# Kernel optimization log

Measured on AMD Instinct MI355X. Metric: run time of the kernel, lower is better.

## Reference

```python
import jax, jax.numpy as jnp
import numpy as np

I_SIZE, H_SIZE, O_SIZE = 3, 128, 3
B, T, A = 512, 50, 64


def _xavier(k, shape):
    fan_out, fan_in = shape
    limit = float(np.sqrt(6.0 / (fan_in + fan_out)))
    return jax.random.uniform(k, shape, minval=-limit, maxval=limit, dtype=jnp.float32)


def setup_inputs() -> dict:
    key = jax.random.key(0)
    ks = jax.random.split(key, 6)
    src = jax.random.normal(ks[0], (B, T, A * I_SIZE), dtype=jnp.float32)
    return {
        "src": src,
        "W_ih_enc": _xavier(ks[1], (H_SIZE, I_SIZE)),
        "W_hh_enc": _xavier(ks[2], (H_SIZE, H_SIZE)),
        "b_ih_enc": jnp.zeros((H_SIZE,), jnp.float32),
        "b_hh_enc": jnp.zeros((H_SIZE,), jnp.float32),
        "W_ih_dec": _xavier(ks[3], (H_SIZE, O_SIZE)),
        "W_hh_dec": _xavier(ks[4], (H_SIZE, H_SIZE)),
        "b_ih_dec": jnp.zeros((H_SIZE,), jnp.float32),
        "b_hh_dec": jnp.zeros((H_SIZE,), jnp.float32),
        "fc_W": _xavier(ks[5], (O_SIZE, H_SIZE)),
        "fc_b": jnp.zeros((O_SIZE,), jnp.float32),
        "pred_len": 12,
    }


def reference(src, W_ih_enc, W_hh_enc, b_ih_enc, b_hh_enc,
              W_ih_dec, W_hh_dec, b_ih_dec, b_hh_dec, fc_W, fc_b, pred_len):
    b, t, f = src.shape
    a = f // I_SIZE
    # (b, t, a*I) -> (t, b*a, I): agents batched together (vectorizes the per-agent loop)
    xs = src.reshape(b, t, a, I_SIZE).transpose(1, 0, 2, 3).reshape(t, b * a, I_SIZE)

    def enc_step(h, x_t):
        h = jnp.tanh(x_t @ W_ih_enc.T + b_ih_enc + h @ W_hh_enc.T + b_hh_enc)
        return h, None

    h0 = jnp.zeros((b * a, H_SIZE), src.dtype)
    h_enc, _ = jax.lax.scan(enc_step, h0, xs)

    # decoder input = last observed position of each agent
    dec_in0 = xs[-1]  # (b*a, I)

    def dec_step(carry, _):
        h, inp = carry
        h = jnp.tanh(inp @ W_ih_dec.T + b_ih_dec + h @ W_hh_dec.T + b_hh_dec)
        pred = h @ fc_W.T + fc_b  # (b*a, O)
        return (h, pred), pred

    _, preds = jax.lax.scan(dec_step, (h_enc, dec_in0), None, length=pred_len)
    # (pred_len, b*a, O) -> (b, pred_len, a*O)
    out = preds.reshape(pred_len, b, a, O_SIZE).transpose(1, 0, 2, 3).reshape(b, pred_len, a * O_SIZE)
    return out
```

## Files before the change

### kernel.cpp

```cpp
#include <hip/hip_runtime.h>
#include <stdint.h>

typedef _Float16 f16x8 __attribute__((ext_vector_type(8)));
typedef float f32x4 __attribute__((ext_vector_type(4)));
typedef unsigned int u32x4 __attribute__((ext_vector_type(4)));

#define T_OBS 50
#define PRED 12

#define DEC_OFF 20480
#define FC_OFF  40960
#define WS_ELEMS 43008

__device__ __forceinline__ int unperm(int k) {
  return (k & 3) | (((k >> 3) & 3) << 2) | (((k >> 2) & 1) << 4) | (k & 0x60);
}

__global__ void prep_kernel(const float* __restrict__ Wih_e, const float* __restrict__ Whh_e,
                            const float* __restrict__ bih_e, const float* __restrict__ bhh_e,
                            const float* __restrict__ Wih_d, const float* __restrict__ Whh_d,
                            const float* __restrict__ bih_d, const float* __restrict__ bhh_d,
                            const float* __restrict__ fcW,
                            unsigned short* __restrict__ ws) {
  int idx = blockIdx.x * 256 + threadIdx.x;
  if (idx >= WS_ELEMS) return;
  float val = 0.0f;
  if (idx < FC_OFF) {
    const bool enc = idx < DEC_OFF;
    const int e = enc ? idx : idx - DEC_OFF;
    const int j = e & 7;
    const int lane = (e >> 3) & 63;
    const int rem = e >> 9;
    const int kt = rem % 5;
    const int t = rem / 5;
    const int n = 16 * t + (lane & 15);
    const int kappa = 32 * kt + ((lane >> 4) << 3) + j;
    const float* Wih = enc ? Wih_e : Wih_d;
    const float* Whh = enc ? Whh_e : Whh_d;
    const float* bih = enc ? bih_e : bih_d;
    const float* bhh = enc ? bhh_e : bhh_d;
    if (kappa < 128)       val = Whh[n * 128 + unperm(kappa)];
    else if (kappa < 131)  val = Wih[n * 3 + (kappa - 128)];
    else if (kappa == 131) val = bih[n] + bhh[n];
  } else {
    const int e = idx - FC_OFF;
    const int j = e & 7;
    const int lane = (e >> 3) & 63;
    const int kt = e >> 9;
    const int o = lane & 15;
    const int kappa = 32 * kt + ((lane >> 4) << 3) + j;
    if (o < 3) val = fcW[o * 128 + unperm(kappa)];
  }
  _Float16 h = (_Float16)val;
  ws[idx] = __builtin_bit_cast(unsigned short, h);
}

__device__ __forceinline__ float tanh_fast(float v) {
  float e = __builtin_amdgcn_exp2f(v * 2.8853900817779268f);
  return __builtin_fmaf(-2.0f, __builtin_amdgcn_rcpf(1.0f + e), 1.0f);
}

__device__ __forceinline__ unsigned int pk2(float a, float b) {
  return __builtin_bit_cast(unsigned int, __builtin_amdgcn_cvt_pkrtz(a, b));
}

__device__ __forceinline__ f16x8 ldfrag(const unsigned short* p) {
  return __builtin_bit_cast(f16x8, *(const u32x4*)p);
}

__device__ __forceinline__ f16x8 mkxf(float a, float b, float c) {
  u32x4 u;
  u[0] = pk2(a, b);
  u[1] = pk2(c, 1.0f);
  u[2] = 0u;
  u[3] = 0u;
  return __builtin_bit_cast(f16x8, u);
}

__global__ __launch_bounds__(256, 3) void traj_kernel(
    const float* __restrict__ src, const unsigned short* __restrict__ ws,
    const float* __restrict__ fcb, float* __restrict__ out) {
  __shared__ unsigned short xch[2][4][2][64][8];

  const int lane = (int)(threadIdx.x & 63u);
  const int w = (int)(threadIdx.x >> 6u);
  const int l15 = lane & 15;
  const int sA = blockIdx.x * 32 + l15;
  const int sB = sA + 16;
  const float* xpA = src + (size_t)(sA >> 6) * (T_OBS * 192) + (sA & 63) * 3;
  const float* xpB = src + (size_t)(sB >> 6) * (T_OBS * 192) + (sB & 63) * 3;

  f16x8 A0[5], A1[5];
  #pragma unroll
  for (int i = 0; i < 5; ++i) {
    const int kt = (i < 4) ? ((w + i) & 3) : 4;
    A0[i] = ldfrag(ws + (size_t)(((2 * w)     * 5 + kt) * 64 + lane) * 8);
    A1[i] = ldfrag(ws + (size_t)(((2 * w + 1) * 5 + kt) * 64 + lane) * 8);
  }

  f16x8 B0[4], B1[4];
  #pragma unroll
  for (int i = 0; i < 4; ++i) {
    u32x4 zz = (u32x4)0u;
    B0[i] = __builtin_bit_cast(f16x8, zz);
    B1[i] = __builtin_bit_cast(f16x8, zz);
  }

  f16x8 xf0 = mkxf(xpA[0], xpA[1], xpA[2]);
  f16x8 xf1 = mkxf(xpB[0], xpB[1], xpB[2]);

  auto rnn_step = [&](int par, f16x8 xfa, f16x8 xfb) {
    const f32x4 z = (f32x4){0.f, 0.f, 0.f, 0.f};
    f32x4 aA = __builtin_amdgcn_mfma_f32_16x16x32_f16(A0[4], xfa, z, 0, 0, 0);
    f32x4 aB = __builtin_amdgcn_mfma_f32_16x16x32_f16(A1[4], xfa, z, 0, 0, 0);
    f32x4 aC = __builtin_amdgcn_mfma_f32_16x16x32_f16(A0[4], xfb, z, 0, 0, 0);
    f32x4 aD = __builtin_amdgcn_mfma_f32_16x16x32_f16(A1[4], xfb, z, 0, 0, 0);
    #pragma unroll
    for (int i = 0; i < 4; ++i) {
      aA = __builtin_amdgcn_mfma_f32_16x16x32_f16(A0[i], B0[i], aA, 0, 0, 0);
      aB = __builtin_amdgcn_mfma_f32_16x16x32_f16(A1[i], B0[i], aB, 0, 0, 0);
      aC = __builtin_amdgcn_mfma_f32_16x16x32_f16(A0[i], B1[i], aC, 0, 0, 0);
      aD = __builtin_amdgcn_mfma_f32_16x16x32_f16(A1[i], B1[i], aD, 0, 0, 0);
    }
    u32x4 F0, F1;
    F0[0] = pk2(tanh_fast(aA[0]), tanh_fast(aA[1]));
    F0[1] = pk2(tanh_fast(aA[2]), tanh_fast(aA[3]));
    F0[2] = pk2(tanh_fast(aB[0]), tanh_fast(aB[1]));
    F0[3] = pk2(tanh_fast(aB[2]), tanh_fast(aB[3]));
    F1[0] = pk2(tanh_fast(aC[0]), tanh_fast(aC[1]));
    F1[1] = pk2(tanh_fast(aC[2]), tanh_fast(aC[3]));
    F1[2] = pk2(tanh_fast(aD[0]), tanh_fast(aD[1]));
    F1[3] = pk2(tanh_fast(aD[2]), tanh_fast(aD[3]));
    *(u32x4*)&xch[par][w][0][lane][0] = F0;
    *(u32x4*)&xch[par][w][1][lane][0] = F1;
    __syncthreads();
    B0[0] = __builtin_bit_cast(f16x8, F0);
    B1[0] = __builtin_bit_cast(f16x8, F1);
    #pragma unroll
    for (int i = 1; i < 4; ++i) {
      B0[i] = ldfrag(&xch[par][(w + i) & 3][0][lane][0]);
      B1[i] = ldfrag(&xch[par][(w + i) & 3][1][lane][0]);
    }
  };

  for (int s = 0; s < T_OBS; ++s) {
    const int t2 = (s < T_OBS - 1) ? s + 1 : s;
    const float na0 = xpA[t2 * 192], na1 = xpA[t2 * 192 + 1], na2 = xpA[t2 * 192 + 2];
    const float nb0 = xpB[t2 * 192], nb1 = xpB[t2 * 192 + 1], nb2 = xpB[t2 * 192 + 2];
    rnn_step(s & 1, xf0, xf1);
    xf0 = mkxf(na0, na1, na2);
    xf1 = mkxf(nb0, nb1, nb2);
  }

  #pragma unroll
  for (int i = 0; i < 5; ++i) {
    const int kt = (i < 4) ? ((w + i) & 3) : 4;
    A0[i] = ldfrag(ws + DEC_OFF + (size_t)(((2 * w)     * 5 + kt) * 64 + lane) * 8);
    A1[i] = ldfrag(ws + DEC_OFF + (size_t)(((2 * w + 1) * 5 + kt) * 64 + lane) * 8);
  }
  f16x8 Afc[4];
  #pragma unroll
  for (int i = 0; i < 4; ++i) {
    const int kt = (w + i) & 3;
    Afc[i] = ldfrag(ws + FC_OFF + (size_t)(kt * 64 + lane) * 8);
  }
  const float fb0 = fcb[0], fb1 = fcb[1], fb2 = fcb[2];

  float* opA = out + (size_t)(sA >> 6) * (PRED * 192) + (sA & 63) * 3;
  float* opB = out + (size_t)(sB >> 6) * (PRED * 192) + (sB & 63) * 3;

  for (int p = 0; p < PRED; ++p) {
    rnn_step(p & 1, xf0, xf1);
    const f32x4 z = (f32x4){0.f, 0.f, 0.f, 0.f};
    f32x4 pA = __builtin_amdgcn_mfma_f32_16x16x32_f16(Afc[0], B0[0], z, 0, 0, 0);
    f32x4 pB = __builtin_amdgcn_mfma_f32_16x16x32_f16(Afc[0], B1[0], z, 0, 0, 0);
    #pragma unroll
    for (int i = 1; i < 4; ++i) {
      pA = __builtin_amdgcn_mfma_f32_16x16x32_f16(Afc[i], B0[i], pA, 0, 0, 0);
      pB = __builtin_amdgcn_mfma_f32_16x16x32_f16(Afc[i], B1[i], pB, 0, 0, 0);
    }
    const float pa0 = pA[0] + fb0, pa1 = pA[1] + fb1, pa2 = pA[2] + fb2;
    const float pb0 = pB[0] + fb0, pb1 = pB[1] + fb1, pb2 = pB[2] + fb2;
    if (w == 0 && lane < 16) {
      opA[p * 192 + 0] = pa0; opA[p * 192 + 1] = pa1; opA[p * 192 + 2] = pa2;
      opB[p * 192 + 0] = pb0; opB[p * 192 + 1] = pb1; opB[p * 192 + 2] = pb2;
    }
    xf0 = mkxf(pa0, pa1, pa2);
    xf1 = mkxf(pb0, pb1, pb2);
  }
}

extern "C" void kernel_launch(void* const* d_in, const int* in_sizes, int n_in,
                              void* d_out, int out_size, void* d_ws, size_t ws_size,
                              hipStream_t stream) {
  const float* src   = (const float*)d_in[0];
  const float* Wih_e = (const float*)d_in[1];
  const float* Whh_e = (const float*)d_in[2];
  const float* bih_e = (const float*)d_in[3];
  const float* bhh_e = (const float*)d_in[4];
  const float* Wih_d = (const float*)d_in[5];
  const float* Whh_d = (const float*)d_in[6];
  const float* bih_d = (const float*)d_in[7];
  const float* bhh_d = (const float*)d_in[8];
  const float* fcW   = (const float*)d_in[9];
  const float* fcb   = (const float*)d_in[10];
  (void)in_sizes; (void)n_in; (void)out_size; (void)ws_size;

  unsigned short* ws = (unsigned short*)d_ws;

  prep_kernel<<<(WS_ELEMS + 255) / 256, 256, 0, stream>>>(
      Wih_e, Whh_e, bih_e, bhh_e, Wih_d, Whh_d, bih_d, bhh_d, fcW, ws);

  traj_kernel<<<1024, 256, 0, stream>>>(src, ws, fcb, (float*)d_out);
}
```

Measured before the change: 99.02 us.

## Keep full recurrent weights in registers per wave, drop LDS exchange and barriers

Each wave now owns 32 sequences and holds all 40 weight fragments in registers, computing the whole hidden state itself. This removes the per-step LDS exchange of hidden fragments and the block-wide barrier. In exchange the grid shrinks to a quarter of the blocks with one wave per SIMD, so latency hiding relies on independent MFMA chains within a wave, and register pressure rises substantially.

```diff
diff --git a/kernel.cpp b/kernel.cpp
--- a/kernel.cpp
+++ b/kernel.cpp
@@ -77,116 +77,107 @@
   return __builtin_bit_cast(f16x8, u);
 }
 
-__global__ __launch_bounds__(256, 3) void traj_kernel(
+__global__ __launch_bounds__(256, 1) void traj_kernel(
     const float* __restrict__ src, const unsigned short* __restrict__ ws,
     const float* __restrict__ fcb, float* __restrict__ out) {
-  __shared__ unsigned short xch[2][4][2][64][8];
-
   const int lane = (int)(threadIdx.x & 63u);
   const int w = (int)(threadIdx.x >> 6u);
-  const int l15 = lane & 15;
-  const int sA = blockIdx.x * 32 + l15;
-  const int sB = sA + 16;
-  const float* xpA = src + (size_t)(sA >> 6) * (T_OBS * 192) + (sA & 63) * 3;
-  const float* xpB = src + (size_t)(sB >> 6) * (T_OBS * 192) + (sB & 63) * 3;
-
-  f16x8 A0[5], A1[5];
-  #pragma unroll
-  for (int i = 0; i < 5; ++i) {
-    const int kt = (i < 4) ? ((w + i) & 3) : 4;
-    A0[i] = ldfrag(ws + (size_t)(((2 * w)     * 5 + kt) * 64 + lane) * 8);
-    A1[i] = ldfrag(ws + (size_t)(((2 * w + 1) * 5 + kt) * 64 + lane) * 8);
-  }
-
-  f16x8 B0[4], B1[4];
+  const int sX = blockIdx.x * 128 + w * 32 + (lane & 15);
+  const int sY = sX + 16;
+  const float* xpX = src + (size_t)(sX >> 6) * (T_OBS * 192) + (sX & 63) * 3;
+  const float* xpY = src + (size_t)(sY >> 6) * (T_OBS * 192) + (sY & 63) * 3;
+
+  f16x8 A[40];
+  #pragma unroll
+  for (int i = 0; i < 40; ++i)
+    A[i] = ldfrag(ws + (size_t)(i * 64 + lane) * 8);
+
+  f16x8 BfX[4], BfY[4];
   #pragma unroll
   for (int i = 0; i < 4; ++i) {
     u32x4 zz = (u32x4)0u;
-    B0[i] = __builtin_bit_cast(f16x8, zz);
-    B1[i] = __builtin_bit_cast(f16x8, zz);
-  }
-
-  f16x8 xf0 = mkxf(xpA[0], xpA[1], xpA[2]);
-  f16x8 xf1 = mkxf(xpB[0], xpB[1], xpB[2]);
-
-  auto rnn_step = [&](int par, f16x8 xfa, f16x8 xfb) {
-    const f32x4 z = (f32x4){0.f, 0.f, 0.f, 0.f};
-    f32x4 aA = __builtin_amdgcn_mfma_f32_16x16x32_f16(A0[4], xfa, z, 0, 0, 0);
-    f32x4 aB = __builtin_amdgcn_mfma_f32_16x16x32_f16(A1[4], xfa, z, 0, 0, 0);
-    f32x4 aC = __builtin_amdgcn_mfma_f32_16x16x32_f16(A0[4], xfb, z, 0, 0, 0);
-    f32x4 aD = __builtin_amdgcn_mfma_f32_16x16x32_f16(A1[4], xfb, z, 0, 0, 0);
-    #pragma unroll
-    for (int i = 0; i < 4; ++i) {
-      aA = __builtin_amdgcn_mfma_f32_16x16x32_f16(A0[i], B0[i], aA, 0, 0, 0);
-      aB = __builtin_amdgcn_mfma_f32_16x16x32_f16(A1[i], B0[i], aB, 0, 0, 0);
-      aC = __builtin_amdgcn_mfma_f32_16x16x32_f16(A0[i], B1[i], aC, 0, 0, 0);
-      aD = __builtin_amdgcn_mfma_f32_16x16x32_f16(A1[i], B1[i], aD, 0, 0, 0);
-    }
-    u32x4 F0, F1;
-    F0[0] = pk2(tanh_fast(aA[0]), tanh_fast(aA[1]));
-    F0[1] = pk2(tanh_fast(aA[2]), tanh_fast(aA[3]));
-    F0[2] = pk2(tanh_fast(aB[0]), tanh_fast(aB[1]));
-    F0[3] = pk2(tanh_fast(aB[2]), tanh_fast(aB[3]));
-    F1[0] = pk2(tanh_fast(aC[0]), tanh_fast(aC[1]));
-    F1[1] = pk2(tanh_fast(aC[2]), tanh_fast(aC[3]));
-    F1[2] = pk2(tanh_fast(aD[0]), tanh_fast(aD[1]));
-    F1[3] = pk2(tanh_fast(aD[2]), tanh_fast(aD[3]));
-    *(u32x4*)&xch[par][w][0][lane][0] = F0;
-    *(u32x4*)&xch[par][w][1][lane][0] = F1;
-    __syncthreads();
-    B0[0] = __builtin_bit_cast(f16x8, F0);
-    B1[0] = __builtin_bit_cast(f16x8, F1);
-    #pragma unroll
-    for (int i = 1; i < 4; ++i) {
-      B0[i] = ldfrag(&xch[par][(w + i) & 3][0][lane][0]);
-      B1[i] = ldfrag(&xch[par][(w + i) & 3][1][lane][0]);
+    BfX[i] = __builtin_bit_cast(f16x8, zz);
+    BfY[i] = __builtin_bit_cast(f16x8, zz);
+  }
+  f16x8 xfX = mkxf(xpX[0], xpX[1], xpX[2]);
+  f16x8 xfY = mkxf(xpY[0], xpY[1], xpY[2]);
+
+  const f32x4 z = (f32x4){0.f, 0.f, 0.f, 0.f};
+  f32x4 aX[8], aY[8];
+
+  auto rnn_step = [&]() {
+    #pragma unroll
+    for (int t = 0; t < 8; ++t) {
+      aX[t] = __builtin_amdgcn_mfma_f32_16x16x32_f16(A[t * 5 + 4], xfX, z, 0, 0, 0);
+      #pragma unroll
+      for (int kt = 0; kt < 4; ++kt)
+        aX[t] = __builtin_amdgcn_mfma_f32_16x16x32_f16(A[t * 5 + kt], BfX[kt], aX[t], 0, 0, 0);
+    }
+    #pragma unroll
+    for (int t = 0; t < 8; ++t) {
+      aY[t] = __builtin_amdgcn_mfma_f32_16x16x32_f16(A[t * 5 + 4], xfY, z, 0, 0, 0);
+      #pragma unroll
+      for (int kt = 0; kt < 4; ++kt)
+        aY[t] = __builtin_amdgcn_mfma_f32_16x16x32_f16(A[t * 5 + kt], BfY[kt], aY[t], 0, 0, 0);
+    }
+    #pragma unroll
+    for (int kt = 0; kt < 4; ++kt) {
+      u32x4 F;
+      F[0] = pk2(tanh_fast(aX[2 * kt][0]),     tanh_fast(aX[2 * kt][1]));
+      F[1] = pk2(tanh_fast(aX[2 * kt][2]),     tanh_fast(aX[2 * kt][3]));
+      F[2] = pk2(tanh_fast(aX[2 * kt + 1][0]), tanh_fast(aX[2 * kt + 1][1]));
+      F[3] = pk2(tanh_fast(aX[2 * kt + 1][2]), tanh_fast(aX[2 * kt + 1][3]));
+      BfX[kt] = __builtin_bit_cast(f16x8, F);
+    }
+    #pragma unroll
+    for (int kt = 0; kt < 4; ++kt) {
+      u32x4 F;
+      F[0] = pk2(tanh_fast(aY[2 * kt][0]),     tanh_fast(aY[2 * kt][1]));
+      F[1] = pk2(tanh_fast(aY[2 * kt][2]),     tanh_fast(aY[2 * kt][3]));
+      F[2] = pk2(tanh_fast(aY[2 * kt + 1][0]), tanh_fast(aY[2 * kt + 1][1]));
+      F[3] = pk2(tanh_fast(aY[2 * kt + 1][2]), tanh_fast(aY[2 * kt + 1][3]));
+      BfY[kt] = __builtin_bit_cast(f16x8, F);
     }
   };
 
   for (int s = 0; s < T_OBS; ++s) {
     const int t2 = (s < T_OBS - 1) ? s + 1 : s;
-    const float na0 = xpA[t2 * 192], na1 = xpA[t2 * 192 + 1], na2 = xpA[t2 * 192 + 2];
-    const float nb0 = xpB[t2 * 192], nb1 = xpB[t2 * 192 + 1], nb2 = xpB[t2 * 192 + 2];
-    rnn_step(s & 1, xf0, xf1);
-    xf0 = mkxf(na0, na1, na2);
-    xf1 = mkxf(nb0, nb1, nb2);
-  }
-
-  #pragma unroll
-  for (int i = 0; i < 5; ++i) {
-    const int kt = (i < 4) ? ((w + i) & 3) : 4;
-    A0[i] = ldfrag(ws + DEC_OFF + (size_t)(((2 * w)     * 5 + kt) * 64 + lane) * 8);
-    A1[i] = ldfrag(ws + DEC_OFF + (size_t)(((2 * w + 1) * 5 + kt) * 64 + lane) * 8);
-  }
+    const float nX0 = xpX[t2 * 192], nX1 = xpX[t2 * 192 + 1], nX2 = xpX[t2 * 192 + 2];
+    const float nY0 = xpY[t2 * 192], nY1 = xpY[t2 * 192 + 1], nY2 = xpY[t2 * 192 + 2];
+    rnn_step();
+    xfX = mkxf(nX0, nX1, nX2);
+    xfY = mkxf(nY0, nY1, nY2);
+  }
+
+  #pragma unroll
+  for (int i = 0; i < 40; ++i)
+    A[i] = ldfrag(ws + DEC_OFF + (size_t)(i * 64 + lane) * 8);
   f16x8 Afc[4];
   #pragma unroll
-  for (int i = 0; i < 4; ++i) {
-    const int kt = (w + i) & 3;
-    Afc[i] = ldfrag(ws + FC_OFF + (size_t)(kt * 64 + lane) * 8);
-  }
+  for (int kt = 0; kt < 4; ++kt)
+    Afc[kt] = ldfrag(ws + FC_OFF + (size_t)(kt * 64 + lane) * 8);
   const float fb0 = fcb[0], fb1 = fcb[1], fb2 = fcb[2];
 
-  float* opA = out + (size_t)(sA >> 6) * (PRED * 192) + (sA & 63) * 3;
-  float* opB = out + (size_t)(sB >> 6) * (PRED * 192) + (sB & 63) * 3;
+  float* opX = out + (size_t)(sX >> 6) * (PRED * 192) + (sX & 63) * 3;
+  float* opY = out + (size_t)(sY >> 6) * (PRED * 192) + (sY & 63) * 3;
 
   for (int p = 0; p < PRED; ++p) {
-    rnn_step(p & 1, xf0, xf1);
-    const f32x4 z = (f32x4){0.f, 0.f, 0.f, 0.f};
-    f32x4 pA = __builtin_amdgcn_mfma_f32_16x16x32_f16(Afc[0], B0[0], z, 0, 0, 0);
-    f32x4 pB = __builtin_amdgcn_mfma_f32_16x16x32_f16(Afc[0], B1[0], z, 0, 0, 0);
-    #pragma unroll
-    for (int i = 1; i < 4; ++i) {
-      pA = __builtin_amdgcn_mfma_f32_16x16x32_f16(Afc[i], B0[i], pA, 0, 0, 0);
-      pB = __builtin_amdgcn_mfma_f32_16x16x32_f16(Afc[i], B1[i], pB, 0, 0, 0);
-    }
-    const float pa0 = pA[0] + fb0, pa1 = pA[1] + fb1, pa2 = pA[2] + fb2;
-    const float pb0 = pB[0] + fb0, pb1 = pB[1] + fb1, pb2 = pB[2] + fb2;
-    if (w == 0 && lane < 16) {
-      opA[p * 192 + 0] = pa0; opA[p * 192 + 1] = pa1; opA[p * 192 + 2] = pa2;
-      opB[p * 192 + 0] = pb0; opB[p * 192 + 1] = pb1; opB[p * 192 + 2] = pb2;
-    }
-    xf0 = mkxf(pa0, pa1, pa2);
-    xf1 = mkxf(pb0, pb1, pb2);
+    rnn_step();
+    f32x4 pX = __builtin_amdgcn_mfma_f32_16x16x32_f16(Afc[0], BfX[0], z, 0, 0, 0);
+    f32x4 pY = __builtin_amdgcn_mfma_f32_16x16x32_f16(Afc[0], BfY[0], z, 0, 0, 0);
+    #pragma unroll
+    for (int kt = 1; kt < 4; ++kt) {
+      pX = __builtin_amdgcn_mfma_f32_16x16x32_f16(Afc[kt], BfX[kt], pX, 0, 0, 0);
+      pY = __builtin_amdgcn_mfma_f32_16x16x32_f16(Afc[kt], BfY[kt], pY, 0, 0, 0);
+    }
+    const float pX0 = pX[0] + fb0, pX1 = pX[1] + fb1, pX2 = pX[2] + fb2;
+    const float pY0 = pY[0] + fb0, pY1 = pY[1] + fb1, pY2 = pY[2] + fb2;
+    if (lane < 16) {
+      opX[p * 192 + 0] = pX0; opX[p * 192 + 1] = pX1; opX[p * 192 + 2] = pX2;
+      opY[p * 192 + 0] = pY0; opY[p * 192 + 1] = pY1; opY[p * 192 + 2] = pY2;
+    }
+    xfX = mkxf(pX0, pX1, pX2);
+    xfY = mkxf(pY0, pY1, pY2);
   }
 }
 
@@ -211,5 +202,5 @@
   prep_kernel<<<(WS_ELEMS + 255) / 256, 256, 0, stream>>>(
       Wih_e, Whh_e, bih_e, bhh_e, Wih_d, Whh_d, bih_d, bhh_d, fcW, ws);
 
-  traj_kernel<<<1024, 256, 0, stream>>>(src, ws, fcb, (float*)d_out);
-}
+  traj_kernel<<<256, 256, 0, stream>>>(src, ws, fcb, (float*)d_out);
+}
```

After: 104.9 us. 5.9% more time.

## Split RNN hidden dimension across two waves per 16-sequence block

Applied to the files above, without the earlier changes.

Each block now handles 16 sequences with 2 wavefronts instead of 32 sequences with 4 wavefronts. Each wave computes 64 hidden units (4 output tiles) over the full K, holding 20 weight fragments in registers, and exchanges only with its partner wave through shared memory. The aim is to cut the LDS reads and the barrier width per step and to launch twice as many smaller blocks. In exchange each wave holds more weight registers and issues more MFMAs per sequence, which may lower occupancy.

```diff
diff --git a/kernel.cpp b/kernel.cpp
--- a/kernel.cpp
+++ b/kernel.cpp
@@ -77,116 +77,114 @@
   return __builtin_bit_cast(f16x8, u);
 }
 
-__global__ __launch_bounds__(256, 3) void traj_kernel(
+__global__ __launch_bounds__(128, 4) void traj_kernel(
     const float* __restrict__ src, const unsigned short* __restrict__ ws,
     const float* __restrict__ fcb, float* __restrict__ out) {
-  __shared__ unsigned short xch[2][4][2][64][8];
+  __shared__ unsigned short xch[2][2][2][64][8];
 
   const int lane = (int)(threadIdx.x & 63u);
   const int w = (int)(threadIdx.x >> 6u);
-  const int l15 = lane & 15;
-  const int sA = blockIdx.x * 32 + l15;
-  const int sB = sA + 16;
-  const float* xpA = src + (size_t)(sA >> 6) * (T_OBS * 192) + (sA & 63) * 3;
-  const float* xpB = src + (size_t)(sB >> 6) * (T_OBS * 192) + (sB & 63) * 3;
-
-  f16x8 A0[5], A1[5];
-  #pragma unroll
-  for (int i = 0; i < 5; ++i) {
-    const int kt = (i < 4) ? ((w + i) & 3) : 4;
-    A0[i] = ldfrag(ws + (size_t)(((2 * w)     * 5 + kt) * 64 + lane) * 8);
-    A1[i] = ldfrag(ws + (size_t)(((2 * w + 1) * 5 + kt) * 64 + lane) * 8);
-  }
-
-  f16x8 B0[4], B1[4];
+  const int seq = blockIdx.x * 16 + (lane & 15);
+  const int b = seq >> 6;
+  const int a = seq & 63;
+
+  f16x8 A[20];
+  #pragma unroll
+  for (int tl = 0; tl < 4; ++tl) {
+    const int t = 4 * w + tl;
+    #pragma unroll
+    for (int lf = 0; lf < 5; ++lf) {
+      const int kt = (lf < 4) ? ((2 * w + lf) & 3) : 4;
+      A[tl * 5 + lf] = ldfrag(ws + (size_t)((t * 5 + kt) * 64 + lane) * 8);
+    }
+  }
+
+  const float* xq = src + (size_t)b * (T_OBS * 192) + a * 3;
+  float x0 = xq[0], x1 = xq[1], x2 = xq[2];
+  xq += 192;
+
+  f16x8 Bl[4];
   #pragma unroll
   for (int i = 0; i < 4; ++i) {
     u32x4 zz = (u32x4)0u;
-    B0[i] = __builtin_bit_cast(f16x8, zz);
-    B1[i] = __builtin_bit_cast(f16x8, zz);
-  }
-
-  f16x8 xf0 = mkxf(xpA[0], xpA[1], xpA[2]);
-  f16x8 xf1 = mkxf(xpB[0], xpB[1], xpB[2]);
-
-  auto rnn_step = [&](int par, f16x8 xfa, f16x8 xfb) {
-    const f32x4 z = (f32x4){0.f, 0.f, 0.f, 0.f};
-    f32x4 aA = __builtin_amdgcn_mfma_f32_16x16x32_f16(A0[4], xfa, z, 0, 0, 0);
-    f32x4 aB = __builtin_amdgcn_mfma_f32_16x16x32_f16(A1[4], xfa, z, 0, 0, 0);
-    f32x4 aC = __builtin_amdgcn_mfma_f32_16x16x32_f16(A0[4], xfb, z, 0, 0, 0);
-    f32x4 aD = __builtin_amdgcn_mfma_f32_16x16x32_f16(A1[4], xfb, z, 0, 0, 0);
-    #pragma unroll
-    for (int i = 0; i < 4; ++i) {
-      aA = __builtin_amdgcn_mfma_f32_16x16x32_f16(A0[i], B0[i], aA, 0, 0, 0);
-      aB = __builtin_amdgcn_mfma_f32_16x16x32_f16(A1[i], B0[i], aB, 0, 0, 0);
-      aC = __builtin_amdgcn_mfma_f32_16x16x32_f16(A0[i], B1[i], aC, 0, 0, 0);
-      aD = __builtin_amdgcn_mfma_f32_16x16x32_f16(A1[i], B1[i], aD, 0, 0, 0);
+    Bl[i] = __builtin_bit_cast(f16x8, zz);
+  }
+  f16x8 xf = mkxf(x0, x1, x2);
+
+  const f32x4 z = (f32x4){0.f, 0.f, 0.f, 0.f};
+
+  auto rnn_step = [&](int par) {
+    f32x4 acc0, acc1, acc2, acc3;
+    acc0 = __builtin_amdgcn_mfma_f32_16x16x32_f16(A[0 * 5 + 4], xf, z, 0, 0, 0);
+    acc1 = __builtin_amdgcn_mfma_f32_16x16x32_f16(A[1 * 5 + 4], xf, z, 0, 0, 0);
+    acc2 = __builtin_amdgcn_mfma_f32_16x16x32_f16(A[2 * 5 + 4], xf, z, 0, 0, 0);
+    acc3 = __builtin_amdgcn_mfma_f32_16x16x32_f16(A[3 * 5 + 4], xf, z, 0, 0, 0);
+    #pragma unroll
+    for (int lf = 0; lf < 4; ++lf) {
+      acc0 = __builtin_amdgcn_mfma_f32_16x16x32_f16(A[0 * 5 + lf], Bl[lf], acc0, 0, 0, 0);
+      acc1 = __builtin_amdgcn_mfma_f32_16x16x32_f16(A[1 * 5 + lf], Bl[lf], acc1, 0, 0, 0);
+      acc2 = __builtin_amdgcn_mfma_f32_16x16x32_f16(A[2 * 5 + lf], Bl[lf], acc2, 0, 0, 0);
+      acc3 = __builtin_amdgcn_mfma_f32_16x16x32_f16(A[3 * 5 + lf], Bl[lf], acc3, 0, 0, 0);
     }
     u32x4 F0, F1;
-    F0[0] = pk2(tanh_fast(aA[0]), tanh_fast(aA[1]));
-    F0[1] = pk2(tanh_fast(aA[2]), tanh_fast(aA[3]));
-    F0[2] = pk2(tanh_fast(aB[0]), tanh_fast(aB[1]));
-    F0[3] = pk2(tanh_fast(aB[2]), tanh_fast(aB[3]));
-    F1[0] = pk2(tanh_fast(aC[0]), tanh_fast(aC[1]));
-    F1[1] = pk2(tanh_fast(aC[2]), tanh_fast(aC[3]));
-    F1[2] = pk2(tanh_fast(aD[0]), tanh_fast(aD[1]));
-    F1[3] = pk2(tanh_fast(aD[2]), tanh_fast(aD[3]));
+    F0[0] = pk2(tanh_fast(acc0[0]), tanh_fast(acc0[1]));
+    F0[1] = pk2(tanh_fast(acc0[2]), tanh_fast(acc0[3]));
+    F0[2] = pk2(tanh_fast(acc1[0]), tanh_fast(acc1[1]));
+    F0[3] = pk2(tanh_fast(acc1[2]), tanh_fast(acc1[3]));
+    F1[0] = pk2(tanh_fast(acc2[0]), tanh_fast(acc2[1]));
+    F1[1] = pk2(tanh_fast(acc2[2]), tanh_fast(acc2[3]));
+    F1[2] = pk2(tanh_fast(acc3[0]), tanh_fast(acc3[1]));
+    F1[3] = pk2(tanh_fast(acc3[2]), tanh_fast(acc3[3]));
     *(u32x4*)&xch[par][w][0][lane][0] = F0;
     *(u32x4*)&xch[par][w][1][lane][0] = F1;
     __syncthreads();
-    B0[0] = __builtin_bit_cast(f16x8, F0);
-    B1[0] = __builtin_bit_cast(f16x8, F1);
-    #pragma unroll
-    for (int i = 1; i < 4; ++i) {
-      B0[i] = ldfrag(&xch[par][(w + i) & 3][0][lane][0]);
-      B1[i] = ldfrag(&xch[par][(w + i) & 3][1][lane][0]);
-    }
+    Bl[0] = __builtin_bit_cast(f16x8, F0);
+    Bl[1] = __builtin_bit_cast(f16x8, F1);
+    Bl[2] = ldfrag(&xch[par][w ^ 1][0][lane][0]);
+    Bl[3] = ldfrag(&xch[par][w ^ 1][1][lane][0]);
   };
 
   for (int s = 0; s < T_OBS; ++s) {
-    const int t2 = (s < T_OBS - 1) ? s + 1 : s;
-    const float na0 = xpA[t2 * 192], na1 = xpA[t2 * 192 + 1], na2 = xpA[t2 * 192 + 2];
-    const float nb0 = xpB[t2 * 192], nb1 = xpB[t2 * 192 + 1], nb2 = xpB[t2 * 192 + 2];
-    rnn_step(s & 1, xf0, xf1);
-    xf0 = mkxf(na0, na1, na2);
-    xf1 = mkxf(nb0, nb1, nb2);
-  }
-
-  #pragma unroll
-  for (int i = 0; i < 5; ++i) {
-    const int kt = (i < 4) ? ((w + i) & 3) : 4;
-    A0[i] = ldfrag(ws + DEC_OFF + (size_t)(((2 * w)     * 5 + kt) * 64 + lane) * 8);
-    A1[i] = ldfrag(ws + DEC_OFF + (size_t)(((2 * w + 1) * 5 + kt) * 64 + lane) * 8);
+    const float nx0 = xq[0], nx1 = xq[1], nx2 = xq[2];
+    xq += (s < T_OBS - 2) ? 192 : 0;
+    rnn_step(s & 1);
+    if (s < T_OBS - 1) xf = mkxf(nx0, nx1, nx2);
+  }
+
+  #pragma unroll
+  for (int tl = 0; tl < 4; ++tl) {
+    const int t = 4 * w + tl;
+    #pragma unroll
+    for (int lf = 0; lf < 5; ++lf) {
+      const int kt = (lf < 4) ? ((2 * w + lf) & 3) : 4;
+      A[tl * 5 + lf] = ldfrag(ws + DEC_OFF + (size_t)((t * 5 + kt) * 64 + lane) * 8);
+    }
   }
   f16x8 Afc[4];
   #pragma unroll
-  for (int i = 0; i < 4; ++i) {
-    const int kt = (w + i) & 3;
-    Afc[i] = ldfrag(ws + FC_OFF + (size_t)(kt * 64 + lane) * 8);
+  for (int lf = 0; lf < 4; ++lf) {
+    const int kt = (2 * w + lf) & 3;
+    Afc[lf] = ldfrag(ws + FC_OFF + (size_t)(kt * 64 + lane) * 8);
   }
   const float fb0 = fcb[0], fb1 = fcb[1], fb2 = fcb[2];
 
-  float* opA = out + (size_t)(sA >> 6) * (PRED * 192) + (sA & 63) * 3;
-  float* opB = out + (size_t)(sB >> 6) * (PRED * 192) + (sB & 63) * 3;
+  float* op = out + (size_t)b * (PRED * 192) + a * 3;
 
   for (int p = 0; p < PRED; ++p) {
-    rnn_step(p & 1, xf0, xf1);
-    const f32x4 z = (f32x4){0.f, 0.f, 0.f, 0.f};
-    f32x4 pA = __builtin_amdgcn_mfma_f32_16x16x32_f16(Afc[0], B0[0], z, 0, 0, 0);
-    f32x4 pB = __builtin_amdgcn_mfma_f32_16x16x32_f16(Afc[0], B1[0], z, 0, 0, 0);
-    #pragma unroll
-    for (int i = 1; i < 4; ++i) {
-      pA = __builtin_amdgcn_mfma_f32_16x16x32_f16(Afc[i], B0[i], pA, 0, 0, 0);
-      pB = __builtin_amdgcn_mfma_f32_16x16x32_f16(Afc[i], B1[i], pB, 0, 0, 0);
-    }
-    const float pa0 = pA[0] + fb0, pa1 = pA[1] + fb1, pa2 = pA[2] + fb2;
-    const float pb0 = pB[0] + fb0, pb1 = pB[1] + fb1, pb2 = pB[2] + fb2;
+    rnn_step(p & 1);
+    f32x4 pf = __builtin_amdgcn_mfma_f32_16x16x32_f16(Afc[0], Bl[0], z, 0, 0, 0);
+    #pragma unroll
+    for (int lf = 1; lf < 4; ++lf)
+      pf = __builtin_amdgcn_mfma_f32_16x16x32_f16(Afc[lf], Bl[lf], pf, 0, 0, 0);
+    const float p0 = pf[0] + fb0;
+    const float p1 = pf[1] + fb1;
+    const float p2 = pf[2] + fb2;
     if (w == 0 && lane < 16) {
-      opA[p * 192 + 0] = pa0; opA[p * 192 + 1] = pa1; opA[p * 192 + 2] = pa2;
-      opB[p * 192 + 0] = pb0; opB[p * 192 + 1] = pb1; opB[p * 192 + 2] = pb2;
-    }
-    xf0 = mkxf(pa0, pa1, pa2);
-    xf1 = mkxf(pb0, pb1, pb2);
+      op[p * 192 + 0] = p0;
+      op[p * 192 + 1] = p1;
+      op[p * 192 + 2] = p2;
+    }
+    xf = mkxf(p0, p1, p2);
   }
 }
 
@@ -211,5 +209,5 @@
   prep_kernel<<<(WS_ELEMS + 255) / 256, 256, 0, stream>>>(
       Wih_e, Whh_e, bih_e, bhh_e, Wih_d, Whh_d, bih_d, bhh_d, fcW, ws);
 
-  traj_kernel<<<1024, 256, 0, stream>>>(src, ws, fcb, (float*)d_out);
-}
+  traj_kernel<<<2048, 128, 0, stream>>>(src, ws, fcb, (float*)d_out);
+}
```

New measurement: 107.8 us. 1.09x slower.
